# Kernel optimization log

Measured on AMD Instinct MI355X. Metric: run time of the kernel, lower is better.

## Reference

```python
import jax, jax.numpy as jnp
import numpy as np

HEAD_DIM = 64  # config['head_dim']
# dropout_prob=0.1 is a no-op in eval mode; reference computes deterministic attention.

def setup_inputs() -> dict:
    key = jax.random.key(0)
    kq, kk, kv = jax.random.split(key, 3)
    shape = (2, 12, 2048, HEAD_DIM)  # [batch, heads, seq, head_dim]
    Q = jax.random.normal(kq, shape, dtype=jnp.float32)
    K = jax.random.normal(kk, shape, dtype=jnp.float32)
    V = jax.random.normal(kv, shape, dtype=jnp.float32)
    return {"Q": Q, "K": K, "V": V}

def reference(Q, K, V):
    # dot = Q @ K^T / sqrt(head_dim); attn = softmax(dot); X = attn @ V
    scale = 1.0 / np.float32(np.sqrt(HEAD_DIM))
    dot = jnp.einsum('bhqd,bhkd->bhqk', Q, K) * scale  # [B,H,S,S]
    attn = jax.nn.softmax(dot, axis=-1)
    X = jnp.einsum('bhqk,bhkd->bhqd', attn, V)
    return X
```

## Files before the change

kernel.cpp:

```cpp
#include <hip/hip_runtime.h>
#include <hip/hip_bf16.h>

typedef __attribute__((ext_vector_type(8))) short bf16x8;
typedef __attribute__((ext_vector_type(4))) float f32x4;
typedef __attribute__((ext_vector_type(4))) unsigned short u16x4;
typedef __attribute__((ext_vector_type(2))) unsigned int u32x2;
typedef __attribute__((ext_vector_type(4))) unsigned int u32x4;
typedef __attribute__((ext_vector_type(4))) _Float16 f16x4;
typedef __attribute__((ext_vector_type(8))) _Float16 f16x8;
typedef __attribute__((ext_vector_type(2))) __fp16 h16x2;
typedef __attribute__((ext_vector_type(4))) __fp16 h16x4;

#define SEQ 2048
#define HD 64
#define BH 24

__device__ __forceinline__ unsigned bfpack(float a, float b) {
  union { float f; unsigned u; } ua, ub; ua.f = a; ub.f = b;
  return __builtin_amdgcn_perm(ub.u + 0x8000u, ua.u + 0x8000u, 0x07060302u);
}
__device__ __forceinline__ unsigned short f2bf(float f) {
  union { float f; unsigned u; } v; v.f = f;
  unsigned r = v.u + 0x7fffu + ((v.u >> 16) & 1u);
  return (unsigned short)(r >> 16);
}

__global__ __launch_bounds__(256) void prep_kv(const float* __restrict__ K,
                                               const float* __restrict__ V,
                                               unsigned* __restrict__ Kb,
                                               _Float16* __restrict__ Vt) {
  __shared__ _Float16 t[64 * 68];
  const int bid = blockIdx.x;
  const int sb = bid >> 3;
  const int bh = (bid & 7) * 3 + (sb >> 5);
  const int k0 = (sb & 31) * 64;
  const int tid = threadIdx.x;

  const float4* ks = (const float4*)(K + ((size_t)bh * SEQ + k0) * HD);
  unsigned* kd = Kb + ((size_t)bh * SEQ + k0) * (HD / 2);
#pragma unroll
  for (int i = 0; i < 4; ++i) {
    int f = tid + i * 256;
    float4 v = ks[f];
    u32x2 o;
    o.x = bfpack(v.x, v.y);
    o.y = bfpack(v.z, v.w);
    *(u32x2*)&kd[f * 2] = o;
  }

  const float4* vs = (const float4*)(V + ((size_t)bh * SEQ + k0) * HD);
#pragma unroll
  for (int i = 0; i < 4; ++i) {
    int f = tid + i * 256;
    int k = f >> 4, cg = f & 15;
    float4 v = vs[k * 16 + cg];
    int dg = cg * 4;
    t[(dg + 0) * 68 + k] = (_Float16)v.x;
    t[(dg + 1) * 68 + k] = (_Float16)v.y;
    t[(dg + 2) * 68 + k] = (_Float16)v.z;
    t[(dg + 3) * 68 + k] = (_Float16)v.w;
  }
  __syncthreads();
  int d = tid >> 2, kg = (tid & 3) * 16;
  _Float16* g = Vt + ((size_t)(bh * 64 + d)) * SEQ + k0 + kg;
#pragma unroll
  for (int r = 0; r < 4; ++r) {
    f16x4 x = *(f16x4*)&t[d * 68 + kg + r * 4];
    *(f16x4*)&g[r * 4] = x;
  }
}

__global__ __launch_bounds__(256, 3) void attn_main(const float* __restrict__ Q,
                                                    const unsigned short* __restrict__ Kb,
                                                    const _Float16* __restrict__ Vt,
                                                    float* __restrict__ O) {
  __shared__ unsigned short kv[3][8192];

  const int tid  = threadIdx.x;
  const int lane = tid & 63;
  const int w    = tid >> 6;
  const int quad = lane >> 4;
  const int n    = lane & 15;

  const int bid = blockIdx.x;
  const int sb = bid >> 3;
  const int bh = (bid & 7) * 3 + (sb >> 5);
  const int q0 = (sb & 31) * 64;

  const float qscale = 0.125f * 1.44269504088896f;

  bf16x8 qf[4][2];
#pragma unroll
  for (int u = 0; u < 4; ++u) {
    const float* qb = Q + ((size_t)bh * SEQ + q0 + u * 16 + n) * HD;
#pragma unroll
    for (int h = 0; h < 2; ++h) {
      float4 a = *(const float4*)(qb + h * 32 + quad * 8);
      float4 b = *(const float4*)(qb + h * 32 + quad * 8 + 4);
      u32x4 pk;
      pk.x = bfpack(a.x * qscale, a.y * qscale);
      pk.y = bfpack(a.z * qscale, a.w * qscale);
      pk.z = bfpack(b.x * qscale, b.y * qscale);
      pk.w = bfpack(b.z * qscale, b.w * qscale);
      qf[u][h] = __builtin_bit_cast(bf16x8, pk);
    }
  }

  const unsigned short* Kbase = Kb + (size_t)bh * SEQ * HD;
  const unsigned short* Vbase = (const unsigned short*)(Vt + (size_t)bh * HD * SEQ);
  const unsigned short* ksrc[2];
  const unsigned short* vsrc[2];
  int soff[2];
#pragma unroll
  for (int i = 0; i < 2; ++i) {
    int s = i * 256 + tid;
    int r = s >> 3, p = s & 7, G = p ^ (r & 7);
    ksrc[i] = Kbase + r * HD + G * 8;
    vsrc[i] = Vbase + (size_t)r * SEQ + G * 8;
    soff[i] = s * 8;
  }

#define DMA_TO(buf_, it_)                                                                 \
  {                                                                                       \
    unsigned short* db_ = &kv[buf_][0];                                                   \
    _Pragma("unroll")                                                                     \
    for (int i_ = 0; i_ < 2; ++i_) {                                                      \
      __builtin_amdgcn_global_load_lds(                                                   \
          (const __attribute__((address_space(1))) void*)(ksrc[i_] + (size_t)(it_) * 4096), \
          (__attribute__((address_space(3))) void*)(db_ + soff[i_]), 16, 0, 0);           \
      __builtin_amdgcn_global_load_lds(                                                   \
          (const __attribute__((address_space(1))) void*)(vsrc[i_] + (size_t)(it_) * 64), \
          (__attribute__((address_space(3))) void*)(db_ + 4096 + soff[i_]), 16, 0, 0);    \
    }                                                                                     \
    asm volatile("" ::: "memory");                                                        \
  }

  f32x4 o[4][4];
#pragma unroll
  for (int dt = 0; dt < 4; ++dt)
#pragma unroll
    for (int u = 0; u < 4; ++u) o[dt][u] = (f32x4){0.f, 0.f, 0.f, 0.f};
  float lsum[4] = {0.f, 0.f, 0.f, 0.f};

  int ro[2];
#pragma unroll
  for (int h = 0; h < 2; ++h) ro[h] = n * 64 + (((h * 4 + quad) ^ (n & 7)) * 8);
  int vo[4];
#pragma unroll
  for (int dt = 0; dt < 4; ++dt)
    vo[dt] = dt * 1024 + n * 64 + (((w * 2 + (quad >> 1)) ^ (n & 7)) * 8) + (quad & 1) * 4;

  u32x4 ppw[4];
  u32x4 vvw[4];

#define QK_SM(buf_, WA_, WB_)                                                             \
  {                                                                                       \
    const unsigned short* kb = &kv[buf_][0];                                              \
    f32x4 s[4] = {{0,0,0,0},{0,0,0,0},{0,0,0,0},{0,0,0,0}};                               \
    _Pragma("unroll")                                                                     \
    for (int h = 0; h < 2; ++h) {                                                         \
      bf16x8 a = *(const bf16x8*)&kb[w * 1024 + ro[h]];                                   \
      _Pragma("unroll")                                                                   \
      for (int u = 0; u < 4; ++u)                                                         \
        s[u] = __builtin_amdgcn_mfma_f32_16x16x32_bf16(a, qf[u][h], s[u], 0, 0, 0);       \
    }                                                                                     \
    _Pragma("unroll")                                                                     \
    for (int u = 0; u < 4; ++u) {                                                         \
      float e0 = __builtin_amdgcn_exp2f(s[u][0]);                                         \
      float e1 = __builtin_amdgcn_exp2f(s[u][1]);                                         \
      float e2 = __builtin_amdgcn_exp2f(s[u][2]);                                         \
      float e3 = __builtin_amdgcn_exp2f(s[u][3]);                                         \
      lsum[u] += (e0 + e1) + (e2 + e3);                                                   \
      h16x2 a_ = __builtin_amdgcn_cvt_pkrtz(e0, e1);                                      \
      h16x2 b_ = __builtin_amdgcn_cvt_pkrtz(e2, e3);                                      \
      ppw[u].WA_ = __builtin_bit_cast(unsigned, a_);                                      \
      ppw[u].WB_ = __builtin_bit_cast(unsigned, b_);                                      \
    }                                                                                     \
  }

#define COMPUTE_EVEN(buf_)                                                                \
  {                                                                                       \
    QK_SM(buf_, x, y);                                                                    \
    const _Float16* vb_ = (const _Float16*)(&kv[buf_][0] + 4096);                         \
    _Pragma("unroll")                                                                     \
    for (int dt = 0; dt < 4; ++dt) {                                                      \
      u32x2 v2 = *(const u32x2*)(vb_ + vo[dt]);                                           \
      vvw[dt].x = v2.x;                                                                   \
      vvw[dt].y = v2.y;                                                                   \
    }                                                                                     \
    asm volatile("s_waitcnt lgkmcnt(0)" ::: "memory");                                    \
  }

#define COMPUTE_ODD(buf_)                                                                 \
  {                                                                                       \
    QK_SM(buf_, z, w);                                                                    \
    const _Float16* vb_ = (const _Float16*)(&kv[buf_][0] + 4096);                         \
    _Pragma("unroll")                                                                     \
    for (int dt = 0; dt < 4; ++dt) {                                                      \
      u32x2 v2 = *(const u32x2*)(vb_ + vo[dt]);                                           \
      vvw[dt].z = v2.x;                                                                   \
      vvw[dt].w = v2.y;                                                                   \
      f16x8 av = __builtin_bit_cast(f16x8, vvw[dt]);                                      \
      _Pragma("unroll")                                                                   \
      for (int u = 0; u < 4; ++u) {                                                       \
        f16x8 pb = __builtin_bit_cast(f16x8, ppw[u]);                                     \
        o[dt][u] = __builtin_amdgcn_mfma_f32_16x16x32_f16(av, pb, o[dt][u], 0, 0, 0);     \
      }                                                                                   \
    }                                                                                     \
  }

  DMA_TO(0, 0);
  DMA_TO(1, 1);

  int bc = 0;
  int bd = 2;
  for (int t = 0; t < 15; ++t) {
    asm volatile("s_waitcnt vmcnt(4)\n\ts_barrier" ::: "memory");
    DMA_TO(bd, 2 * t + 2);
    COMPUTE_EVEN(bc);
    bc = (bc == 2) ? 0 : bc + 1;
    bd = (bd == 2) ? 0 : bd + 1;
    asm volatile("s_waitcnt vmcnt(4)\n\ts_barrier" ::: "memory");
    DMA_TO(bd, 2 * t + 3);
    COMPUTE_ODD(bc);
    bc = (bc == 2) ? 0 : bc + 1;
    bd = (bd == 2) ? 0 : bd + 1;
  }
  asm volatile("s_waitcnt vmcnt(4)\n\ts_barrier" ::: "memory");
  COMPUTE_EVEN(bc);
  bc = (bc == 2) ? 0 : bc + 1;
  asm volatile("s_waitcnt vmcnt(0)\n\ts_barrier" ::: "memory");
  COMPUTE_ODD(bc);

#undef DMA_TO
#undef QK_SM
#undef COMPUTE_EVEN
#undef COMPUTE_ODD

#pragma unroll
  for (int u = 0; u < 4; ++u) {
    lsum[u] += __shfl_xor(lsum[u], 16);
    lsum[u] += __shfl_xor(lsum[u], 32);
  }

  float* red = (float*)&kv[0][0];
  float* lred = red + 2 * 4096;

  __syncthreads();
  if (w & 1) {
    int s = w >> 1;
#pragma unroll
    for (int dt = 0; dt < 4; ++dt)
#pragma unroll
      for (int u = 0; u < 4; ++u)
        *(f32x4*)&red[s * 4096 + (dt * 4 + u) * 256 + lane * 4] = o[dt][u];
#pragma unroll
    for (int u = 0; u < 4; ++u) lred[s * 256 + u * 64 + lane] = lsum[u];
  }
  __syncthreads();
  if (!(w & 1)) {
    int s = w >> 1;
#pragma unroll
    for (int dt = 0; dt < 4; ++dt)
#pragma unroll
      for (int u = 0; u < 4; ++u)
        o[dt][u] += *(f32x4*)&red[s * 4096 + (dt * 4 + u) * 256 + lane * 4];
#pragma unroll
    for (int u = 0; u < 4; ++u) lsum[u] += lred[s * 256 + u * 64 + lane];
  }
  __syncthreads();
  if (w == 2) {
#pragma unroll
    for (int dt = 0; dt < 4; ++dt)
#pragma unroll
      for (int u = 0; u < 4; ++u)
        *(f32x4*)&red[4096 + (dt * 4 + u) * 256 + lane * 4] = o[dt][u];
#pragma unroll
    for (int u = 0; u < 4; ++u) lred[256 + u * 64 + lane] = lsum[u];
  }
  __syncthreads();
  if (w == 0) {
#pragma unroll
    for (int dt = 0; dt < 4; ++dt)
#pragma unroll
      for (int u = 0; u < 4; ++u)
        o[dt][u] += *(f32x4*)&red[4096 + (dt * 4 + u) * 256 + lane * 4];
#pragma unroll
    for (int u = 0; u < 4; ++u) {
      float inv = 1.0f / (lsum[u] + lred[256 + u * 64 + lane]);
      float* og = O + ((size_t)bh * SEQ + q0 + u * 16 + n) * HD + quad * 4;
#pragma unroll
      for (int dt = 0; dt < 4; ++dt) {
        f32x4 r = o[dt][u];
        r.x *= inv; r.y *= inv; r.z *= inv; r.w *= inv;
        *(f32x4*)(og + dt * 16) = r;
      }
    }
  }
}

#define F_QT 128
#define F_KT 64
#define F_LD 72

__global__ __launch_bounds__(512) void attn_fwd(const float* __restrict__ Q,
                                                const float* __restrict__ K,
                                                const float* __restrict__ V,
                                                float* __restrict__ O) {
  __shared__ unsigned short sm[(F_QT + F_KT + HD + 8 * 16) * F_LD];
  unsigned short* Qs = sm;
  unsigned short* Ks = Qs + F_QT * F_LD;
  unsigned short* Vt = Ks + F_KT * F_LD;
  unsigned short* Ps = Vt + HD * F_LD;

  const int tid = threadIdx.x, lane = tid & 63, wv = tid >> 6;
  const int quad = lane >> 4, n = lane & 15;
  const int bh = blockIdx.y, q0 = blockIdx.x * F_QT;
  const float* Qg = Q + ((size_t)bh * SEQ + q0) * HD;
  const float* Kg = K + (size_t)bh * SEQ * HD;
  const float* Vg = V + (size_t)bh * SEQ * HD;
  float* Og = O + ((size_t)bh * SEQ + q0) * HD;
  const float qscale = 0.125f * 1.44269504088896f;

#pragma unroll
  for (int i = 0; i < 4; ++i) {
    int f = tid + i * 512;
    int row = f >> 4, cg = f & 15;
    float4 qv = ((const float4*)Qg)[row * 16 + cg];
    u16x4 h;
    h.x = f2bf(qv.x * qscale); h.y = f2bf(qv.y * qscale);
    h.z = f2bf(qv.z * qscale); h.w = f2bf(qv.w * qscale);
    *(u16x4*)&Qs[row * F_LD + cg * 4] = h;
  }
  __syncthreads();
  bf16x8 qf0 = *(const bf16x8*)&Qs[(wv * 16 + n) * F_LD + quad * 8];
  bf16x8 qf1 = *(const bf16x8*)&Qs[(wv * 16 + n) * F_LD + 32 + quad * 8];
  f32x4 o[4] = {{0,0,0,0},{0,0,0,0},{0,0,0,0},{0,0,0,0}};
  float mrow[4] = {-1e30f,-1e30f,-1e30f,-1e30f};
  float lrow[4] = {0.f,0.f,0.f,0.f};
  unsigned short* Pw = Ps + wv * 16 * F_LD;

  for (int it = 0; it < SEQ / F_KT; ++it) {
    __syncthreads();
    const float* Ktg = Kg + (size_t)it * F_KT * HD;
    const float* Vtg = Vg + (size_t)it * F_KT * HD;
#pragma unroll
    for (int i = 0; i < 2; ++i) {
      int f = tid + i * 512;
      int row = f >> 4, cg = f & 15;
      float4 kvv = ((const float4*)Ktg)[row * 16 + cg];
      u16x4 hk;
      hk.x = f2bf(kvv.x); hk.y = f2bf(kvv.y); hk.z = f2bf(kvv.z); hk.w = f2bf(kvv.w);
      *(u16x4*)&Ks[row * F_LD + cg * 4] = hk;
      float4 vv = ((const float4*)Vtg)[row * 16 + cg];
      Vt[(cg * 4 + 0) * F_LD + row] = f2bf(vv.x);
      Vt[(cg * 4 + 1) * F_LD + row] = f2bf(vv.y);
      Vt[(cg * 4 + 2) * F_LD + row] = f2bf(vv.z);
      Vt[(cg * 4 + 3) * F_LD + row] = f2bf(vv.w);
    }
    __syncthreads();
    f32x4 s[4];
#pragma unroll
    for (int t = 0; t < 4; ++t) {
      bf16x8 b0 = *(const bf16x8*)&Ks[(t * 16 + n) * F_LD + quad * 8];
      bf16x8 b1 = *(const bf16x8*)&Ks[(t * 16 + n) * F_LD + 32 + quad * 8];
      f32x4 c = {0,0,0,0};
      c = __builtin_amdgcn_mfma_f32_16x16x32_bf16(qf0, b0, c, 0, 0, 0);
      c = __builtin_amdgcn_mfma_f32_16x16x32_bf16(qf1, b1, c, 0, 0, 0);
      s[t] = c;
    }
    float mnew[4], alpha[4], rsum[4];
#pragma unroll
    for (int r = 0; r < 4; ++r) {
      float ml = fmaxf(fmaxf(s[0][r], s[1][r]), fmaxf(s[2][r], s[3][r]));
      ml = fmaxf(ml, __shfl_xor(ml, 1));
      ml = fmaxf(ml, __shfl_xor(ml, 2));
      ml = fmaxf(ml, __shfl_xor(ml, 4));
      ml = fmaxf(ml, __shfl_xor(ml, 8));
      mnew[r] = fmaxf(mrow[r], ml);
      alpha[r] = __builtin_amdgcn_exp2f(mrow[r] - mnew[r]);
      mrow[r] = mnew[r];
      rsum[r] = 0.f;
    }
#pragma unroll
    for (int t = 0; t < 4; ++t)
#pragma unroll
      for (int r = 0; r < 4; ++r) {
        float p = __builtin_amdgcn_exp2f(s[t][r] - mnew[r]);
        rsum[r] += p;
        Pw[(quad * 4 + r) * F_LD + t * 16 + n] = f2bf(p);
      }
#pragma unroll
    for (int r = 0; r < 4; ++r) {
      float rs = rsum[r];
      rs += __shfl_xor(rs, 1); rs += __shfl_xor(rs, 2);
      rs += __shfl_xor(rs, 4); rs += __shfl_xor(rs, 8);
      lrow[r] = lrow[r] * alpha[r] + rs;
      o[0][r] *= alpha[r]; o[1][r] *= alpha[r];
      o[2][r] *= alpha[r]; o[3][r] *= alpha[r];
    }
    asm volatile("s_waitcnt lgkmcnt(0)" ::: "memory");
    bf16x8 p0 = *(const bf16x8*)&Pw[n * F_LD + quad * 8];
    bf16x8 p1 = *(const bf16x8*)&Pw[n * F_LD + 32 + quad * 8];
#pragma unroll
    for (int t = 0; t < 4; ++t) {
      bf16x8 v0 = *(const bf16x8*)&Vt[(t * 16 + n) * F_LD + quad * 8];
      bf16x8 v1 = *(const bf16x8*)&Vt[(t * 16 + n) * F_LD + 32 + quad * 8];
      o[t] = __builtin_amdgcn_mfma_f32_16x16x32_bf16(p0, v0, o[t], 0, 0, 0);
      o[t] = __builtin_amdgcn_mfma_f32_16x16x32_bf16(p1, v1, o[t], 0, 0, 0);
    }
  }
  float inv[4];
#pragma unroll
  for (int r = 0; r < 4; ++r) inv[r] = 1.0f / lrow[r];
#pragma unroll
  for (int t = 0; t < 4; ++t)
#pragma unroll
    for (int r = 0; r < 4; ++r)
      Og[(wv * 16 + quad * 4 + r) * HD + t * 16 + n] = o[t][r] * inv[r];
}

extern "C" void kernel_launch(void* const* d_in, const int* in_sizes, int n_in,
                              void* d_out, int out_size, void* d_ws, size_t ws_size,
                              hipStream_t stream) {
  const float* Q = (const float*)d_in[0];
  const float* K = (const float*)d_in[1];
  const float* V = (const float*)d_in[2];
  float* O = (float*)d_out;

  const size_t mat = (size_t)BH * SEQ * HD;
  const size_t need = 2 * mat * sizeof(unsigned short);

  if (ws_size >= need) {
    unsigned short* Kb = (unsigned short*)d_ws;
    _Float16* Vt = (_Float16*)(Kb + mat);
    prep_kv<<<dim3(SEQ / 64 * BH), 256, 0, stream>>>(K, V, (unsigned*)Kb, Vt);
    attn_main<<<dim3(BH * SEQ / 64), 256, 0, stream>>>(Q, Kb, Vt, O);
  } else {
    attn_fwd<<<dim3(SEQ / F_QT, BH), 512, 0, stream>>>(Q, K, V, O);
  }
}
```

Before: 120.0 us.

## Defer V loads to odd step and restructure triple-buffer rotation

Even steps now only compute QK and softmax numerators. Both V halves are read from LDS in the odd step, directly before the PV MFMAs, so the V fragment no longer has to stay in registers across the barrier and the lgkmcnt wait after the even step goes away. The buffer rotation changes so the next DMA is issued only after an extra lgkmcnt wait and barrier following the odd compute. This is meant to cut register pressure and a mid-step wait, but it adds a barrier per iteration and issues one DMA later, which shortens prefetch lead time.

```diff
diff --git a/kernel.cpp b/kernel.cpp
--- a/kernel.cpp
+++ b/kernel.cpp
@@ -151,7 +151,6 @@
     vo[dt] = dt * 1024 + n * 64 + (((w * 2 + (quad >> 1)) ^ (n & 7)) * 8) + (quad & 1) * 4;
 
   u32x4 ppw[4];
-  u32x4 vvw[4];
 
 #define QK_SM(buf_, WA_, WB_)                                                             \
   {                                                                                       \
@@ -178,29 +177,23 @@
     }                                                                                     \
   }
 
-#define COMPUTE_EVEN(buf_)                                                                \
+#define COMPUTE_EVEN(bufA_)                                                               \
   {                                                                                       \
-    QK_SM(buf_, x, y);                                                                    \
-    const _Float16* vb_ = (const _Float16*)(&kv[buf_][0] + 4096);                         \
+    QK_SM(bufA_, x, y);                                                                   \
+  }
+
+#define COMPUTE_ODD(bufA_, bufB_)                                                         \
+  {                                                                                       \
+    QK_SM(bufB_, z, w);                                                                   \
+    const _Float16* va_ = (const _Float16*)(&kv[bufA_][0] + 4096);                        \
+    const _Float16* vb_ = (const _Float16*)(&kv[bufB_][0] + 4096);                        \
     _Pragma("unroll")                                                                     \
     for (int dt = 0; dt < 4; ++dt) {                                                      \
-      u32x2 v2 = *(const u32x2*)(vb_ + vo[dt]);                                           \
-      vvw[dt].x = v2.x;                                                                   \
-      vvw[dt].y = v2.y;                                                                   \
-    }                                                                                     \
-    asm volatile("s_waitcnt lgkmcnt(0)" ::: "memory");                                    \
-  }
-
-#define COMPUTE_ODD(buf_)                                                                 \
-  {                                                                                       \
-    QK_SM(buf_, z, w);                                                                    \
-    const _Float16* vb_ = (const _Float16*)(&kv[buf_][0] + 4096);                         \
-    _Pragma("unroll")                                                                     \
-    for (int dt = 0; dt < 4; ++dt) {                                                      \
-      u32x2 v2 = *(const u32x2*)(vb_ + vo[dt]);                                           \
-      vvw[dt].z = v2.x;                                                                   \
-      vvw[dt].w = v2.y;                                                                   \
-      f16x8 av = __builtin_bit_cast(f16x8, vvw[dt]);                                      \
+      u32x2 vA2 = *(const u32x2*)(va_ + vo[dt]);                                          \
+      u32x2 vB2 = *(const u32x2*)(vb_ + vo[dt]);                                          \
+      u32x4 vv;                                                                           \
+      vv.x = vA2.x; vv.y = vA2.y; vv.z = vB2.x; vv.w = vB2.y;                             \
+      f16x8 av = __builtin_bit_cast(f16x8, vv);                                           \
       _Pragma("unroll")                                                                   \
       for (int u = 0; u < 4; ++u) {                                                       \
         f16x8 pb = __builtin_bit_cast(f16x8, ppw[u]);                                     \
@@ -212,25 +205,21 @@
   DMA_TO(0, 0);
   DMA_TO(1, 1);
 
-  int bc = 0;
-  int bd = 2;
+  int b0 = 0, b1 = 1, b2 = 2;
   for (int t = 0; t < 15; ++t) {
     asm volatile("s_waitcnt vmcnt(4)\n\ts_barrier" ::: "memory");
-    DMA_TO(bd, 2 * t + 2);
-    COMPUTE_EVEN(bc);
-    bc = (bc == 2) ? 0 : bc + 1;
-    bd = (bd == 2) ? 0 : bd + 1;
+    DMA_TO(b2, 2 * t + 2);
+    COMPUTE_EVEN(b0);
     asm volatile("s_waitcnt vmcnt(4)\n\ts_barrier" ::: "memory");
-    DMA_TO(bd, 2 * t + 3);
-    COMPUTE_ODD(bc);
-    bc = (bc == 2) ? 0 : bc + 1;
-    bd = (bd == 2) ? 0 : bd + 1;
+    COMPUTE_ODD(b0, b1);
+    asm volatile("s_waitcnt lgkmcnt(0)\n\ts_barrier" ::: "memory");
+    DMA_TO(b0, 2 * t + 3);
+    int tmp = b2; b2 = b1; b1 = b0; b0 = tmp;
   }
   asm volatile("s_waitcnt vmcnt(4)\n\ts_barrier" ::: "memory");
-  COMPUTE_EVEN(bc);
-  bc = (bc == 2) ? 0 : bc + 1;
+  COMPUTE_EVEN(b0);
   asm volatile("s_waitcnt vmcnt(0)\n\ts_barrier" ::: "memory");
-  COMPUTE_ODD(bc);
+  COMPUTE_ODD(b0, b1);
 
 #undef DMA_TO
 #undef QK_SM
```

Measured after the change: 117.9 us. About the same (-1.7%).
